# Kernel optimization log

Measured on AMD Instinct MI355X. Metric: run time of the kernel, lower is better.

The kernel has to match this reference:

```python
import jax, jax.numpy as jnp
import numpy as np
import math

INPUT_DIM = 256
HIDDEN_DIM = 128  # per-head dim
NUM_HEAD = 8
N = 1024          # seq len == variables
BATCH = 8
C = HIDDEN_DIM * NUM_HEAD  # 1024


def setup_inputs() -> dict:
    key = jax.random.key(0)
    ks = jax.random.split(key, 11)
    s = 0.02
    return {
        "x": jax.random.normal(ks[0], (BATCH, N, INPUT_DIM), dtype=jnp.float32),
        "B_bias": jax.random.normal(ks[1], (N, N), dtype=jnp.float32),
        "wq_w": jax.random.normal(ks[2], (INPUT_DIM, C), dtype=jnp.float32) * s,
        "wq_b": jax.random.normal(ks[3], (C,), dtype=jnp.float32) * s,
        "wk_w": jax.random.normal(ks[4], (INPUT_DIM, C), dtype=jnp.float32) * s,
        "wk_b": jax.random.normal(ks[5], (C,), dtype=jnp.float32) * s,
        "wv_w": jax.random.normal(ks[6], (INPUT_DIM, C), dtype=jnp.float32) * s,
        "wv_b": jax.random.normal(ks[7], (C,), dtype=jnp.float32) * s,
        "proj_w": jax.random.normal(ks[8], (C, HIDDEN_DIM), dtype=jnp.float32) * s,
        "proj_b": jax.random.normal(ks[9], (HIDDEN_DIM,), dtype=jnp.float32) * s,
    }


def reference(x, B_bias, wq_w, wq_b, wk_w, wk_b, wv_w, wv_b, proj_w, proj_b):
    B, n, _ = x.shape
    sdk = jnp.float32(math.sqrt(HIDDEN_DIM))
    # projections -> [B, N, C], split heads -> [B, H, N, h]
    def heads(y):
        return y.reshape(B, n, NUM_HEAD, HIDDEN_DIM).transpose(0, 2, 1, 3)
    q = heads(x @ wq_w + wq_b)
    k = heads(x @ wk_w + wk_b)
    v = heads(x @ wv_w + wv_b)
    # scores [B, H, N, N] with learned additive bias (broadcast over B, H)
    scores = jnp.einsum("bhnd,bhmd->bhnm", q, k) / sdk + B_bias
    attn = jax.nn.softmax(scores, axis=-1)
    out = jnp.einsum("bhnm,bhmd->bhnd", attn, v)  # [B, H, N, h]
    out = out.transpose(0, 2, 1, 3).reshape(B, n, C)
    return out @ proj_w + proj_b
```

## Files before the change

kernel.cpp:

```cpp
#include <hip/hip_runtime.h>
#include <math.h>

#define SEQ  1024
#define IND  256
#define CC   1024
#define NH   8
#define HD   128
#define BH   64

typedef __bf16 bf16x8 __attribute__((ext_vector_type(8)));
typedef __bf16 bf16x4 __attribute__((ext_vector_type(4)));
typedef float  f32x4  __attribute__((ext_vector_type(4)));
typedef unsigned short u16;

static constexpr float RSDK = 0.08838834764831845f;

__device__ __forceinline__ u16 f2bf(float f) {
    unsigned int u = __float_as_uint(f);
    u += 0x7fffu + ((u >> 16) & 1u);
    return (u16)(u >> 16);
}

__device__ __forceinline__ unsigned cvt_pk_bf16(float lo, float hi) {
    unsigned r;
    asm("v_cvt_pk_bf16_f32 %0, %1, %2" : "=v"(r) : "v"(lo), "v"(hi));
    return r;
}

__device__ __forceinline__ bf16x8 ld8_cvt(const float* p) {
    float4 lo = *(const float4*)p;
    float4 hi = *(const float4*)(p + 4);
    union { unsigned u[4]; bf16x8 v; } c8;
    c8.u[0] = cvt_pk_bf16(lo.x, lo.y);
    c8.u[1] = cvt_pk_bf16(lo.z, lo.w);
    c8.u[2] = cvt_pk_bf16(hi.x, hi.y);
    c8.u[3] = cvt_pk_bf16(hi.z, hi.w);
    return c8.v;
}

__global__ __launch_bounds__(256) void prep_kernel(
    const float* __restrict__ w0, const float* __restrict__ w1, const float* __restrict__ w2,
    u16* __restrict__ o0, u16* __restrict__ o1, u16* __restrict__ o2,
    const float* __restrict__ pw, u16* __restrict__ pT)
{
    __shared__ float tile[32][33];
    const int id = blockIdx.x;

    const float* in; u16* out; int R, C, c0, r0;
    if (id < 768) {
        const int z = id >> 8;
        const int rem2 = id & 255;
        in  = (z == 0) ? w0 : (z == 1) ? w1 : w2;
        out = (z == 0) ? o0 : (z == 1) ? o1 : o2;
        R = IND; C = CC;
        c0 = (rem2 & 31) * 32;
        r0 = (rem2 >> 5) * 32;
    } else {
        const int rem = id - 768;
        in = pw; out = pT;
        R = CC; C = HD;
        c0 = (rem & 3) * 32;
        r0 = (rem >> 2) * 32;
    }

    const int row = threadIdx.x >> 3, col4 = (threadIdx.x & 7) * 4;
    float4 v = *(const float4*)&in[(size_t)(r0 + row) * C + c0 + col4];
    tile[row][col4 + 0] = v.x; tile[row][col4 + 1] = v.y;
    tile[row][col4 + 2] = v.z; tile[row][col4 + 3] = v.w;
    __syncthreads();
    ushort4 o;
    o.x = f2bf(tile[col4 + 0][row]);
    o.y = f2bf(tile[col4 + 1][row]);
    o.z = f2bf(tile[col4 + 2][row]);
    o.w = f2bf(tile[col4 + 3][row]);
    *(ushort4*)&out[(size_t)(c0 + row) * R + r0 + col4] = o;
}

#define QKV_LDW 72
__global__ __launch_bounds__(256) void qkv_kernel(
    const float* __restrict__ x,
    const u16* __restrict__ wT0, const u16* __restrict__ wT1, const u16* __restrict__ wT2,
    const float* __restrict__ b0, const float* __restrict__ b1, const float* __restrict__ b2,
    u16* __restrict__ q_out, u16* __restrict__ k_out, u16* __restrict__ vt_out)
{
    const int mat = blockIdx.z;
    const u16* wT  = (mat == 0) ? wT0 : (mat == 1) ? wT1 : wT2;
    const float* wb = (mat == 0) ? b0 : (mat == 1) ? b1 : b2;
    const float scale = (mat == 0) ? RSDK : 1.0f;

    __shared__ __align__(16) u16 As[128 * QKV_LDW];
    __shared__ __align__(16) u16 Bs[128 * QKV_LDW];

    const int tid = threadIdx.x;
    const int lane = tid & 63, wave = tid >> 6;
    const int ln = lane & 15, quad = lane >> 4;
    const int m0 = blockIdx.x * 128;
    const int n0 = blockIdx.y * 128;
    const int wm = (wave & 1) * 64;
    const int wn = (wave >> 1) * 64;

    f32x4 acc[4][4];
    #pragma unroll
    for (int mb = 0; mb < 4; ++mb)
        #pragma unroll
        for (int nb = 0; nb < 4; ++nb)
            #pragma unroll
            for (int r = 0; r < 4; ++r) acc[mb][nb][r] = 0.0f;

    const int r8 = tid >> 3, pb8 = tid & 7;

    const float* ag = x + (size_t)(m0 + r8) * IND + pb8 * 8;
    const u16*   bg = wT + (size_t)(n0 + r8) * IND + pb8 * 8;

    bf16x8 pa[4], pbv[4];
    #pragma unroll
    for (int c = 0; c < 4; ++c) {
        pa[c]  = ld8_cvt(ag + (size_t)c * 32 * IND);
        pbv[c] = *(const bf16x8*)(bg + (size_t)c * 32 * IND);
    }

    for (int kt = 0; kt < 4; ++kt) {
        __syncthreads();
        #pragma unroll
        for (int c = 0; c < 4; ++c) {
            *(bf16x8*)(As + (size_t)(c * 32 + r8) * QKV_LDW + pb8 * 8) = pa[c];
            *(bf16x8*)(Bs + (size_t)(c * 32 + r8) * QKV_LDW + pb8 * 8) = pbv[c];
        }
        __syncthreads();
        if (kt < 3) {
            #pragma unroll
            for (int c = 0; c < 4; ++c) {
                pa[c]  = ld8_cvt(ag + (size_t)c * 32 * IND + (kt + 1) * 64);
                pbv[c] = *(const bf16x8*)(bg + (size_t)c * 32 * IND + (kt + 1) * 64);
            }
        }
        #pragma unroll
        for (int ks = 0; ks < 2; ++ks) {
            bf16x8 af[4], bf[4];
            #pragma unroll
            for (int mb = 0; mb < 4; ++mb)
                af[mb] = *(const bf16x8*)(As + (size_t)(wm + mb * 16 + ln) * QKV_LDW
                                             + (ks * 4 + quad) * 8);
            #pragma unroll
            for (int nb = 0; nb < 4; ++nb)
                bf[nb] = *(const bf16x8*)(Bs + (size_t)(wn + nb * 16 + ln) * QKV_LDW
                                             + (ks * 4 + quad) * 8);
            if (mat != 2) {
                #pragma unroll
                for (int mb = 0; mb < 4; ++mb)
                    #pragma unroll
                    for (int nb = 0; nb < 4; ++nb)
                        acc[mb][nb] = __builtin_amdgcn_mfma_f32_16x16x32_bf16(
                            bf[nb], af[mb], acc[mb][nb], 0, 0, 0);
            } else {
                #pragma unroll
                for (int mb = 0; mb < 4; ++mb)
                    #pragma unroll
                    for (int nb = 0; nb < 4; ++nb)
                        acc[mb][nb] = __builtin_amdgcn_mfma_f32_16x16x32_bf16(
                            af[mb], bf[nb], acc[mb][nb], 0, 0, 0);
            }
        }
    }

    if (mat != 2) {
        u16* outp = (mat == 0) ? q_out : k_out;
        const int h = n0 >> 7;
        float4 bv[4];
        #pragma unroll
        for (int nb = 0; nb < 4; ++nb)
            bv[nb] = *(const float4*)&wb[n0 + wn + nb * 16 + quad * 4];
        #pragma unroll
        for (int mb = 0; mb < 4; ++mb) {
            const int m = m0 + wm + mb * 16 + ln;
            const int b = m >> 10, tok = m & 1023;
            u16* orow = outp + ((size_t)(b * NH + h) * SEQ + tok) * HD;
            #pragma unroll
            for (int nb = 0; nb < 4; ++nb) {
                const int d0 = wn + nb * 16 + quad * 4;
                ushort4 o;
                o.x = f2bf((acc[mb][nb][0] + bv[nb].x) * scale);
                o.y = f2bf((acc[mb][nb][1] + bv[nb].y) * scale);
                o.z = f2bf((acc[mb][nb][2] + bv[nb].z) * scale);
                o.w = f2bf((acc[mb][nb][3] + bv[nb].w) * scale);
                *(ushort4*)&orow[d0] = o;
            }
        }
    } else {
        #pragma unroll
        for (int nb = 0; nb < 4; ++nb) {
            const int c = n0 + wn + nb * 16 + ln;
            const float bv = wb[c];
            const int h = c >> 7, d = c & 127;
            #pragma unroll
            for (int mb = 0; mb < 4; ++mb) {
                const int m = m0 + wm + mb * 16 + quad * 4;
                const int b = m >> 10, tok0 = m & 1023;
                ushort4 o;
                o.x = f2bf(acc[mb][nb][0] + bv);
                o.y = f2bf(acc[mb][nb][1] + bv);
                o.z = f2bf(acc[mb][nb][2] + bv);
                o.w = f2bf(acc[mb][nb][3] + bv);
                *(ushort4*)&vt_out[((size_t)(b * NH + h) * HD + d) * SEQ + tok0] = o;
            }
        }
    }
}

#define KVB    32
#define KS_LDW 136
#define VS_LDW 40
__global__ __launch_bounds__(256, 2) void attn_kernel(
    const u16* __restrict__ Q, const u16* __restrict__ K,
    const u16* __restrict__ Vt, const float* __restrict__ bias,
    u16* __restrict__ aout)
{
    __shared__ __align__(16) u16 Ks[KVB * KS_LDW];
    __shared__ __align__(16) u16 Vs[128 * VS_LDW];

    const int tid = threadIdx.x;
    const int lane = tid & 63, wave = tid >> 6;
    const int ln = lane & 15, quad = lane >> 4;
    const int bh = blockIdx.x;
    const int q0 = blockIdx.y * 128 + wave * 32;

    bf16x8 qf[2][4];
    #pragma unroll
    for (int mb = 0; mb < 2; ++mb) {
        const u16* qp = Q + ((size_t)bh * SEQ + q0 + mb * 16 + ln) * HD + quad * 8;
        #pragma unroll
        for (int ks = 0; ks < 4; ++ks) qf[mb][ks] = *(const bf16x8*)(qp + ks * 32);
    }

    f32x4 Oa[2][8];
    #pragma unroll
    for (int mb = 0; mb < 2; ++mb)
        #pragma unroll
        for (int db = 0; db < 8; ++db)
            #pragma unroll
            for (int r = 0; r < 4; ++r) Oa[mb][db][r] = 0.0f;
    float l_loc[2] = {0.0f, 0.0f};

    const u16* Kg0 = K  + (size_t)bh * SEQ * HD;
    const u16* Vg0 = Vt + (size_t)bh * HD * SEQ;
    const float* brow0 = bias + (size_t)(q0 + ln) * SEQ + quad * 4;
    const float* brow1 = brow0 + (size_t)16 * SEQ;

    const int r16 = tid >> 4, pb16 = tid & 15;
    const int r4  = tid >> 2, pb4  = tid & 3;

    const u16* kg = Kg0 + (size_t)r16 * HD + pb16 * 8;
    const u16* vg = Vg0 + (size_t)r4 * SEQ + pb4 * 8;

    bf16x8 kp[2], vp[2];
    #pragma unroll
    for (int c = 0; c < 2; ++c) {
        kp[c] = *(const bf16x8*)(kg + (size_t)c * 16 * HD);
        vp[c] = *(const bf16x8*)(vg + (size_t)c * 64 * SEQ);
    }

    float4 bpre[2][2];
    #pragma unroll
    for (int mb = 0; mb < 2; ++mb)
        #pragma unroll
        for (int nb = 0; nb < 2; ++nb)
            bpre[mb][nb] = *(const float4*)((mb ? brow1 : brow0) + nb * 16);

    for (int kt = 0; kt < 32; ++kt) {
        __syncthreads();
        #pragma unroll
        for (int c = 0; c < 2; ++c) {
            *(bf16x8*)(Ks + (size_t)(c * 16 + r16) * KS_LDW + pb16 * 8) = kp[c];
            *(bf16x8*)(Vs + (size_t)(c * 64 + r4) * VS_LDW + pb4 * 8)   = vp[c];
        }
        __syncthreads();

        if (kt < 31) {
            #pragma unroll
            for (int c = 0; c < 2; ++c) {
                kp[c] = *(const bf16x8*)(kg + (size_t)(kt + 1) * KVB * HD + (size_t)c * 16 * HD);
                vp[c] = *(const bf16x8*)(vg + (size_t)c * 64 * SEQ + (kt + 1) * KVB);
            }
        }

        float p8[2][2][4];
        #pragma unroll
        for (int nb = 0; nb < 2; ++nb) {
            const u16* kr = Ks + (size_t)(nb * 16 + ln) * KS_LDW;
            bf16x8 kf[4];
            #pragma unroll
            for (int ks = 0; ks < 4; ++ks)
                kf[ks] = *(const bf16x8*)(kr + (ks * 4 + quad) * 8);
            #pragma unroll
            for (int mb = 0; mb < 2; ++mb) {
                f32x4 s;
                #pragma unroll
                for (int r = 0; r < 4; ++r) s[r] = 0.0f;
                __builtin_amdgcn_s_setprio(1);
                #pragma unroll
                for (int ks = 0; ks < 4; ++ks)
                    s = __builtin_amdgcn_mfma_f32_16x16x32_bf16(kf[ks], qf[mb][ks], s, 0, 0, 0);
                __builtin_amdgcn_s_setprio(0);
                #pragma unroll
                for (int r = 0; r < 4; ++r) {
                    const float p = __expf(s[r] + bpre[mb][nb][r]);
                    l_loc[mb] += p;
                    p8[mb][nb][r] = p;
                }
            }
        }

        if (kt < 31) {
            #pragma unroll
            for (int mb = 0; mb < 2; ++mb)
                #pragma unroll
                for (int nb = 0; nb < 2; ++nb)
                    bpre[mb][nb] = *(const float4*)((mb ? brow1 : brow0)
                                                    + (kt + 1) * KVB + nb * 16);
        }

        bf16x8 af[2];
        #pragma unroll
        for (int mb = 0; mb < 2; ++mb) {
            unsigned x0 = cvt_pk_bf16(p8[mb][0][0], p8[mb][0][1]);
            unsigned x1 = cvt_pk_bf16(p8[mb][0][2], p8[mb][0][3]);
            unsigned y0 = cvt_pk_bf16(p8[mb][1][0], p8[mb][1][1]);
            unsigned y1 = cvt_pk_bf16(p8[mb][1][2], p8[mb][1][3]);
            asm("v_permlane32_swap_b32 %0, %1" : "+v"(x0), "+v"(y0));
            asm("v_permlane32_swap_b32 %0, %1" : "+v"(x1), "+v"(y1));
            asm("v_permlane16_swap_b32 %0, %1" : "+v"(x0), "+v"(y0));
            asm("v_permlane16_swap_b32 %0, %1" : "+v"(x1), "+v"(y1));
            union { unsigned u[4]; bf16x8 v; } afu;
            afu.u[0] = x0; afu.u[1] = x1; afu.u[2] = y0; afu.u[3] = y1;
            af[mb] = afu.v;
        }

        __builtin_amdgcn_s_setprio(1);
        #pragma unroll
        for (int db = 0; db < 8; ++db) {
            bf16x8 vf = *(const bf16x8*)(Vs + (size_t)(db * 16 + ln) * VS_LDW + quad * 8);
            #pragma unroll
            for (int mb = 0; mb < 2; ++mb)
                Oa[mb][db] = __builtin_amdgcn_mfma_f32_16x16x32_bf16(
                    af[mb], vf, Oa[mb][db], 0, 0, 0);
        }
        __builtin_amdgcn_s_setprio(0);
    }

    const int b = bh >> 3, h = bh & 7;
    #pragma unroll
    for (int mb = 0; mb < 2; ++mb) {
        float ltot = l_loc[mb];
        ltot += __shfl_xor(ltot, 16);
        ltot += __shfl_xor(ltot, 32);
        #pragma unroll
        for (int r = 0; r < 4; ++r) {
            const float inv = 1.0f / __shfl(ltot, quad * 4 + r);
            const int tok = q0 + mb * 16 + quad * 4 + r;
            u16* op = aout + ((size_t)(b * SEQ + tok)) * CC + h * HD + ln;
            #pragma unroll
            for (int db = 0; db < 8; ++db) op[db * 16] = f2bf(Oa[mb][db][r] * inv);
        }
    }
}

#define PJ_LDW 1032
__global__ __launch_bounds__(256) void proj_kernel(
    const u16* __restrict__ A, const u16* __restrict__ pT,
    const float* __restrict__ pb, float* __restrict__ out)
{
    __shared__ __align__(16) u16 As16[16 * PJ_LDW];
    __shared__ float Rs[3][16 * 132];
    const int tid = threadIdx.x;
    const int lane = tid & 63, kh = tid >> 6;
    const int ln = lane & 15, quad = lane >> 4;
    const int m0 = blockIdx.x * 16;

    {
        const int row = tid >> 7;
        const int col = (tid & 127) * 8;
        #pragma unroll
        for (int p = 0; p < 8; ++p) {
            const int r = p * 2 + row;
            *(bf16x8*)&As16[(size_t)r * PJ_LDW + col] =
                *(const bf16x8*)&A[(size_t)(m0 + r) * CC + col];
        }
    }
    __syncthreads();

    f32x4 acc[8];
    #pragma unroll
    for (int nb = 0; nb < 8; ++nb)
        #pragma unroll
        for (int r = 0; r < 4; ++r) acc[nb][r] = 0.0f;

    const u16* ap = As16 + (size_t)ln * PJ_LDW + kh * 256 + quad * 8;
    const u16* bp = pT + (size_t)ln * CC + kh * 256 + quad * 8;

    #pragma unroll
    for (int kt = 0; kt < 8; ++kt) {
        bf16x8 af = *(const bf16x8*)(ap + kt * 32);
        #pragma unroll
        for (int nb = 0; nb < 8; ++nb) {
            bf16x8 bf = *(const bf16x8*)(bp + (size_t)nb * 16 * CC + kt * 32);
            acc[nb] = __builtin_amdgcn_mfma_f32_16x16x32_bf16(af, bf, acc[nb], 0, 0, 0);
        }
    }

    if (kh > 0) {
        #pragma unroll
        for (int nb = 0; nb < 8; ++nb)
            #pragma unroll
            for (int r = 0; r < 4; ++r)
                Rs[kh - 1][(quad * 4 + r) * 132 + nb * 16 + ln] = acc[nb][r];
    }
    __syncthreads();
    if (kh == 0) {
        #pragma unroll
        for (int nb = 0; nb < 8; ++nb) {
            const int c = nb * 16 + ln;
            const float bv = pb[c];
            #pragma unroll
            for (int r = 0; r < 4; ++r) {
                const int ri = (quad * 4 + r) * 132 + c;
                out[(size_t)(m0 + quad * 4 + r) * HD + c] =
                    acc[nb][r] + Rs[0][ri] + Rs[1][ri] + Rs[2][ri] + bv;
            }
        }
    }
}

extern "C" void kernel_launch(void* const* d_in, const int* in_sizes, int n_in,
                              void* d_out, int out_size, void* d_ws, size_t ws_size,
                              hipStream_t stream)
{
    const float* x    = (const float*)d_in[0];
    const float* bias = (const float*)d_in[1];
    const float* wq   = (const float*)d_in[2];
    const float* wqb  = (const float*)d_in[3];
    const float* wk   = (const float*)d_in[4];
    const float* wkb  = (const float*)d_in[5];
    const float* wv   = (const float*)d_in[6];
    const float* wvb  = (const float*)d_in[7];
    const float* pw   = (const float*)d_in[8];
    const float* pb   = (const float*)d_in[9];
    float* out = (float*)d_out;

    u16* ws = (u16*)d_ws;
    size_t off = 0;
    u16* wqT = ws + off; off += (size_t)CC * IND;
    u16* wkT = ws + off; off += (size_t)CC * IND;
    u16* wvT = ws + off; off += (size_t)CC * IND;
    u16* pT  = ws + off; off += (size_t)HD * CC;
    u16* Qw  = ws + off; off += (size_t)BH * SEQ * HD;
    u16* Kw  = ws + off; off += (size_t)BH * SEQ * HD;
    u16* Vtw = ws + off; off += (size_t)BH * HD * SEQ;
    u16* Aw  = ws + off; off += (size_t)8192 * CC;

    prep_kernel<<<896, 256, 0, stream>>>(wq, wk, wv, wqT, wkT, wvT, pw, pT);
    qkv_kernel<<<dim3(64, 8, 3), 256, 0, stream>>>(
        x, wqT, wkT, wvT, wqb, wkb, wvb, Qw, Kw, Vtw);
    attn_kernel<<<dim3(64, 8), 256, 0, stream>>>(Qw, Kw, Vtw, bias, Aw);
    proj_kernel<<<512, 256, 0, stream>>>(Aw, pT, pb, out);
}
```

Measured before the change: 177.7 us.

## Software-pipeline attention loop: overlap QK/exp of next tile with PV of previous

Restructures the attention KV loop into a two-stage software pipeline. V tiles are double-buffered in LDS so the PV MFMAs for tile kt-1 can be issued after the QK MFMAs and exp of tile kt, with the P-transpose deferred. The aim is to interleave the exp/VALU work with matrix-core work and hide latency. It costs an extra V buffer in LDS and more live registers (two P fragment sets), which may pressure occupancy at the 2-block launch bound.

```diff
diff --git a/kernel.cpp b/kernel.cpp
--- a/kernel.cpp
+++ b/kernel.cpp
@@ -216,7 +216,7 @@
     u16* __restrict__ aout)
 {
     __shared__ __align__(16) u16 Ks[KVB * KS_LDW];
-    __shared__ __align__(16) u16 Vs[128 * VS_LDW];
+    __shared__ __align__(16) u16 Vs[2][128 * VS_LDW];
 
     const int tid = threadIdx.x;
     const int lane = tid & 63, wave = tid >> 6;
@@ -266,24 +266,9 @@
         for (int nb = 0; nb < 2; ++nb)
             bpre[mb][nb] = *(const float4*)((mb ? brow1 : brow0) + nb * 16);
 
-    for (int kt = 0; kt < 32; ++kt) {
-        __syncthreads();
-        #pragma unroll
-        for (int c = 0; c < 2; ++c) {
-            *(bf16x8*)(Ks + (size_t)(c * 16 + r16) * KS_LDW + pb16 * 8) = kp[c];
-            *(bf16x8*)(Vs + (size_t)(c * 64 + r4) * VS_LDW + pb4 * 8)   = vp[c];
-        }
-        __syncthreads();
-
-        if (kt < 31) {
-            #pragma unroll
-            for (int c = 0; c < 2; ++c) {
-                kp[c] = *(const bf16x8*)(kg + (size_t)(kt + 1) * KVB * HD + (size_t)c * 16 * HD);
-                vp[c] = *(const bf16x8*)(vg + (size_t)c * 64 * SEQ + (kt + 1) * KVB);
-            }
-        }
-
-        float p8[2][2][4];
+    bf16x8 afA[2], afB[2];
+
+    auto qk_exp = [&](const int kt, float p8[2][2][4]) {
         #pragma unroll
         for (int nb = 0; nb < 2; ++nb) {
             const u16* kr = Ks + (size_t)(nb * 16 + ln) * KS_LDW;
@@ -309,7 +294,6 @@
                 }
             }
         }
-
         if (kt < 31) {
             #pragma unroll
             for (int mb = 0; mb < 2; ++mb)
@@ -318,8 +302,9 @@
                     bpre[mb][nb] = *(const float4*)((mb ? brow1 : brow0)
                                                     + (kt + 1) * KVB + nb * 16);
         }
-
-        bf16x8 af[2];
+    };
+
+    auto transpose_p = [&](const float p8[2][2][4], bf16x8 af[2]) {
         #pragma unroll
         for (int mb = 0; mb < 2; ++mb) {
             unsigned x0 = cvt_pk_bf16(p8[mb][0][0], p8[mb][0][1]);
@@ -334,18 +319,64 @@
             afu.u[0] = x0; afu.u[1] = x1; afu.u[2] = y0; afu.u[3] = y1;
             af[mb] = afu.v;
         }
-
+    };
+
+    auto pv = [&](const bf16x8 af[2], const u16* vsb) {
         __builtin_amdgcn_s_setprio(1);
         #pragma unroll
         for (int db = 0; db < 8; ++db) {
-            bf16x8 vf = *(const bf16x8*)(Vs + (size_t)(db * 16 + ln) * VS_LDW + quad * 8);
+            bf16x8 vf = *(const bf16x8*)(vsb + (size_t)(db * 16 + ln) * VS_LDW + quad * 8);
             #pragma unroll
             for (int mb = 0; mb < 2; ++mb)
                 Oa[mb][db] = __builtin_amdgcn_mfma_f32_16x16x32_bf16(
                     af[mb], vf, Oa[mb][db], 0, 0, 0);
         }
         __builtin_amdgcn_s_setprio(0);
-    }
+    };
+
+    for (int it = 0; it < 16; ++it) {
+        {
+            const int kt = 2 * it;
+            __syncthreads();
+            #pragma unroll
+            for (int c = 0; c < 2; ++c) {
+                *(bf16x8*)(Ks + (size_t)(c * 16 + r16) * KS_LDW + pb16 * 8)   = kp[c];
+                *(bf16x8*)(Vs[0] + (size_t)(c * 64 + r4) * VS_LDW + pb4 * 8)  = vp[c];
+            }
+            __syncthreads();
+            #pragma unroll
+            for (int c = 0; c < 2; ++c) {
+                kp[c] = *(const bf16x8*)(kg + (size_t)(kt + 1) * KVB * HD + (size_t)c * 16 * HD);
+                vp[c] = *(const bf16x8*)(vg + (size_t)c * 64 * SEQ + (kt + 1) * KVB);
+            }
+            float p8[2][2][4];
+            qk_exp(kt, p8);
+            if (it > 0) pv(afB, Vs[1]);
+            transpose_p(p8, afA);
+        }
+        {
+            const int kt = 2 * it + 1;
+            __syncthreads();
+            #pragma unroll
+            for (int c = 0; c < 2; ++c) {
+                *(bf16x8*)(Ks + (size_t)(c * 16 + r16) * KS_LDW + pb16 * 8)   = kp[c];
+                *(bf16x8*)(Vs[1] + (size_t)(c * 64 + r4) * VS_LDW + pb4 * 8)  = vp[c];
+            }
+            __syncthreads();
+            if (it < 15) {
+                #pragma unroll
+                for (int c = 0; c < 2; ++c) {
+                    kp[c] = *(const bf16x8*)(kg + (size_t)(kt + 1) * KVB * HD + (size_t)c * 16 * HD);
+                    vp[c] = *(const bf16x8*)(vg + (size_t)c * 64 * SEQ + (kt + 1) * KVB);
+                }
+            }
+            float p8[2][2][4];
+            qk_exp(kt, p8);
+            pv(afA, Vs[0]);
+            transpose_p(p8, afB);
+        }
+    }
+    pv(afB, Vs[1]);
 
     const int b = bh >> 3, h = bh & 7;
     #pragma unroll
```

New measurement: 179.9 us. About the same (+1.2%).
